# Optimization experiments

Measured on AMD Instinct MI355X. Metric: run time of the kernel, lower is better.

The kernel has to match this reference:

```python
import jax, jax.numpy as jnp
import numpy as np

B, N, D = 256, 128, 200   # batch, node tokens, descriptor count (d_desc)
DG, DT, DK, H = 256, 256, 256, 4
DH = DK // H
EPS = 1e-5


def _ln(x, g, b):
    mu = jnp.mean(x, -1, keepdims=True)
    v = jnp.var(x, -1, keepdims=True)
    return (x - mu) * jax.lax.rsqrt(v + EPS) * g + b


def _mh_attn(Q, K, V, key_pad_mask):
    # Q:(B,Tq,DK) K,V:(B,Tk,DK) -> ctx:(B,Tq,DK), scores/attn:(B,H,Tq,Tk)
    Bq, Tq, _ = Q.shape
    Tk = K.shape[1]
    Qh = Q.reshape(Bq, Tq, H, DH)
    Kh = K.reshape(Bq, Tk, H, DH)
    Vh = V.reshape(Bq, Tk, H, DH)
    scores = jnp.einsum('bqhd,bkhd->bhqk', Qh, Kh) / (DH ** 0.5)
    if key_pad_mask is not None:
        scores = jnp.where(key_pad_mask[:, None, None, :], -jnp.inf, scores)
    attn = jax.nn.softmax(scores, axis=-1)
    ctx = jnp.einsum('bhqk,bkhd->bqhd', attn, Vh).reshape(Bq, Tq, DK)
    return ctx, scores, attn


def setup_inputs() -> dict:
    key = jax.random.key(0)
    ks = jax.random.split(key, 20)
    def p(i, shape, s=0.05):
        return jax.random.normal(ks[i], shape, jnp.float32) * s
    return dict(
        node_tokens=jax.random.normal(ks[0], (B, N, DG), jnp.float32),
        desc=jax.random.normal(ks[1], (B, D), jnp.float32),
        node_pad_mask=jax.random.randint(ks[2], (B, N), 0, 2).astype(bool),
        id_emb=p(3, (D, DT)),
        val_w1=p(4, (1, DT // 2)), val_b1=jnp.zeros(DT // 2, jnp.float32),
        val_w2=p(5, (DT // 2, DT)), val_b2=jnp.zeros(DT, jnp.float32),
        tok_ln_g=jnp.ones(DT, jnp.float32), tok_ln_b=jnp.zeros(DT, jnp.float32),
        ln_node_g=jnp.ones(DG, jnp.float32), ln_node_b=jnp.zeros(DG, jnp.float32),
        ln_desc_g=jnp.ones(DT, jnp.float32), ln_desc_b=jnp.zeros(DT, jnp.float32),
        Wq_g=p(6, (DG, DK)), bq_g=jnp.zeros(DK, jnp.float32),
        Wk_g=p(7, (DT, DK)), bk_g=jnp.zeros(DK, jnp.float32),
        Wv_g=p(8, (DT, DK)), bv_g=jnp.zeros(DK, jnp.float32),
        Wq_d=p(9, (DT, DK)), bq_d=jnp.zeros(DK, jnp.float32),
        Wk_d=p(10, (DG, DK)), bk_d=jnp.zeros(DK, jnp.float32),
        Wv_d=p(11, (DG, DK)), bv_d=jnp.zeros(DK, jnp.float32),
        proj_node_w=p(12, (DG, DK)), proj_node_b=jnp.zeros(DK, jnp.float32),
        proj_desc_w=p(13, (DT, DK)), proj_desc_b=jnp.zeros(DK, jnp.float32),
        ln_out_g_g=jnp.ones(DK, jnp.float32), ln_out_g_b=jnp.zeros(DK, jnp.float32),
        ln_out_d_g=jnp.ones(DK, jnp.float32), ln_out_d_b=jnp.zeros(DK, jnp.float32),
    )


def reference(node_tokens, desc, node_pad_mask, id_emb, val_w1, val_b1, val_w2, val_b2,
              tok_ln_g, tok_ln_b, ln_node_g, ln_node_b, ln_desc_g, ln_desc_b,
              Wq_g, bq_g, Wk_g, bk_g, Wv_g, bv_g, Wq_d, bq_d, Wk_d, bk_d, Wv_d, bv_d,
              proj_node_w, proj_node_b, proj_desc_w, proj_desc_b,
              ln_out_g_g, ln_out_g_b, ln_out_d_g, ln_out_d_b):
    # Descriptor tokenizer: per-scalar value MLP + id embedding + LN
    h = jax.nn.relu(desc[..., None] @ val_w1 + val_b1)      # (B,D,DT/2)
    val_emb = h @ val_w2 + val_b2                            # (B,D,DT)
    desc_tks = _ln(val_emb + id_emb, tok_ln_g, tok_ln_b)     # (B,D,DT)

    node_in = _ln(node_tokens, ln_node_g, ln_node_b)
    desc_in = _ln(desc_tks, ln_desc_g, ln_desc_b)

    # nodes attend to desc (no key mask)
    ctx_g, scores_g, attn_g = _mh_attn(node_in @ Wq_g + bq_g,
                                       desc_in @ Wk_g + bk_g,
                                       desc_in @ Wv_g + bv_g, None)
    out_g_tokens = _ln(node_tokens @ proj_node_w + proj_node_b + ctx_g,
                       ln_out_g_g, ln_out_g_b)               # (B,N,DK)
    valid = (~node_pad_mask)[..., None].astype(out_g_tokens.dtype)
    denom = jnp.clip(valid.sum(axis=1), 1.0)
    g_vec = (out_g_tokens * valid).sum(axis=1) / denom       # (B,DK)

    # desc attends to nodes (node pad mask on keys)
    ctx_d, scores_d, attn_d = _mh_attn(desc_in @ Wq_d + bq_d,
                                       node_in @ Wk_d + bk_d,
                                       node_in @ Wv_d + bv_d, node_pad_mask)
    out_d_tokens = _ln(desc_tks @ proj_desc_w + proj_desc_b + ctx_d,
                       ln_out_d_g, ln_out_d_b)               # (B,D,DK)
    d_vec = out_d_tokens.mean(axis=1)                        # (B,DK)

    return (g_vec, d_vec, out_g_tokens, out_d_tokens, scores_g, attn_g, scores_d, attn_d)
```

## Files before the change

### kernel.cpp

```cpp
#include <hip/hip_runtime.h>
#include <cmath>
#include <cfloat>

#define BB 256
#define NN 128
#define DD 200
#define CH 256
#define NH 4
#define QKVS 768

#define BF16_SAFE_MAX 3.0e38f

typedef __attribute__((ext_vector_type(8))) __bf16 bf16x8;
typedef __attribute__((ext_vector_type(4))) __bf16 bf16x4;
typedef __attribute__((ext_vector_type(2))) __bf16 bf16x2;
typedef __attribute__((ext_vector_type(4))) float f32x4;

__device__ __forceinline__ float finclamp(float x) {
  return fminf(fmaxf(x, -BF16_SAFE_MAX), BF16_SAFE_MAX);
}

#define GLOAD_LDS16(gp, lp)                                                    \
  __builtin_amdgcn_global_load_lds(                                            \
      (const __attribute__((address_space(1))) void*)(gp),                     \
      (__attribute__((address_space(3))) void*)(lp), 16, 0, 0)

__device__ __forceinline__ void wred2(float& s, float& ss) {
  #pragma unroll
  for (int o = 1; o < 64; o <<= 1) {
    s += __shfl_xor(s, o);
    ss += __shfl_xor(ss, o);
  }
}

struct W9 { const float* p[9]; };
__global__ __launch_bounds__(256)
void mhca_wconv9(W9 w, __bf16* __restrict__ wt) {
  const int z = blockIdx.z;
  const int K = (z == 0) ? 128 : 256;
  if ((int)blockIdx.x * 64 >= K) return;
  __shared__ float t[64][65];
  const float* W = w.p[z];
  __bf16* Wt = wt + (size_t)z * 65536;
  const int k0 = blockIdx.x * 64, n0 = blockIdx.y * 64;
  const int c = threadIdx.x & 63, r0 = threadIdx.x >> 6;
  #pragma unroll
  for (int r = r0; r < 64; r += 4)
    t[r][c] = W[(size_t)(k0 + r) * 256 + n0 + c];
  __syncthreads();
  #pragma unroll
  for (int r = r0; r < 64; r += 4)
    Wt[(size_t)(n0 + r) * K + k0 + c] = (__bf16)t[c][r];
}

__global__ __launch_bounds__(256)
void mhca_gemm_tok(const float* __restrict__ desc, const float* __restrict__ w1,
                   const float* __restrict__ b1, const __bf16* __restrict__ Wt,
                   const float* __restrict__ bias, __bf16* __restrict__ C) {
  constexpr int K = 128;
  __shared__ char lds[2][2][16384];
  const int tid = threadIdx.x;
  const int lane = tid & 63, w = tid >> 6;
  const int n0 = blockIdx.x * 128, m0 = blockIdx.y * 128;
  const int c = lane & 15, g = lane >> 4;
  const int wr = w >> 1, wc = w & 1;

  const bool isA = (w < 2);
  const int half = isA ? w : (w - 2);
  const char* gsrcB = (const char*)Wt + (size_t)(n0 + half * 64) * (K * 2);
  const int lrow = lane >> 3, s8 = lane & 7;
  const int ksw = (s8 ^ lrow) << 4;

  f32x4 acc[4][4];
  #pragma unroll
  for (int mt = 0; mt < 4; ++mt)
    #pragma unroll
    for (int nt = 0; nt < 4; ++nt) acc[mt][nt] = (f32x4){0.f, 0.f, 0.f, 0.f};

  auto stageA = [&](int buf, int kt) {
    char* Ab = &lds[buf][0][half * 8192];
    const int kk = kt * 64 + s8 * 8;
    float4 wa = *(const float4*)&w1[kk];
    float4 wb = *(const float4*)&w1[kk + 4];
    float4 ba = *(const float4*)&b1[kk];
    float4 bb = *(const float4*)&b1[kk + 4];
    #pragma unroll
    for (int i = 0; i < 8; ++i) {
      const float dv = desc[m0 + half * 64 + i * 8 + lrow];
      bf16x8 av;
      av[0] = (__bf16)fmaxf(dv * wa.x + ba.x, 0.f);
      av[1] = (__bf16)fmaxf(dv * wa.y + ba.y, 0.f);
      av[2] = (__bf16)fmaxf(dv * wa.z + ba.z, 0.f);
      av[3] = (__bf16)fmaxf(dv * wa.w + ba.w, 0.f);
      av[4] = (__bf16)fmaxf(dv * wb.x + bb.x, 0.f);
      av[5] = (__bf16)fmaxf(dv * wb.y + bb.y, 0.f);
      av[6] = (__bf16)fmaxf(dv * wb.z + bb.z, 0.f);
      av[7] = (__bf16)fmaxf(dv * wb.w + bb.w, 0.f);
      *(bf16x8*)(Ab + (i * 8 + lrow) * 128 + ksw) = av;
    }
  };
  auto stageB = [&](int buf, int kt) {
    char* ld = &lds[buf][1][half * 8192];
    const char* gs = gsrcB + kt * 128;
    #pragma unroll
    for (int i = 0; i < 8; ++i)
      GLOAD_LDS16(gs + (size_t)(i * 8 + lrow) * (K * 2) + ksw, ld + i * 1024);
  };

  if (isA) stageA(0, 0); else stageB(0, 0);
  __syncthreads();

  int cur = 0;
  #pragma unroll
  for (int kt = 0; kt < 2; ++kt) {
    if (kt + 1 < 2) { if (isA) stageA(cur ^ 1, 1); else stageB(cur ^ 1, 1); }
    const char* A  = lds[cur][0];
    const char* Bt = lds[cur][1];
    #pragma unroll
    for (int kc = 0; kc < 2; ++kc) {
      const int kb = (kc * 64 + g * 16) ^ ((c & 7) << 4);
      bf16x8 a[4], bv[4];
      #pragma unroll
      for (int mt = 0; mt < 4; ++mt)
        a[mt] = *(const bf16x8*)(A + (wr * 64 + mt * 16 + c) * 128 + kb);
      #pragma unroll
      for (int nt = 0; nt < 4; ++nt)
        bv[nt] = *(const bf16x8*)(Bt + (wc * 64 + nt * 16 + c) * 128 + kb);
      #pragma unroll
      for (int mt = 0; mt < 4; ++mt)
        #pragma unroll
        for (int nt = 0; nt < 4; ++nt)
          acc[mt][nt] = __builtin_amdgcn_mfma_f32_16x16x32_bf16(
              a[mt], bv[nt], acc[mt][nt], 0, 0, 0);
    }
    __syncthreads();
    cur ^= 1;
  }

  #pragma unroll
  for (int nt = 0; nt < 4; ++nt) {
    const int n = n0 + wc * 64 + nt * 16 + c;
    const float bn = bias[n];
    #pragma unroll
    for (int mt = 0; mt < 4; ++mt)
      #pragma unroll
      for (int r = 0; r < 4; ++r) {
        const int m = m0 + wr * 64 + mt * 16 + g * 4 + r;
        C[(size_t)m * CH + n] = (__bf16)(acc[mt][nt][r] + bn);
      }
  }
}

struct G4 {
  const __bf16* X[4]; const __bf16* Wt[4];
  const float* bia[4][3]; __bf16* C[4];
};
__global__ __launch_bounds__(256)
void mhca_gemm4(G4 a) {
  constexpr int K = 256;
  const int y = blockIdx.y;
  int side, my, xlim, SC;
  if (y < 400)      { side = 0; my = y;       xlim = 6; SC = QKVS; }
  else if (y < 656) { side = 1; my = y - 400; xlim = 6; SC = QKVS; }
  else if (y < 912) { side = 2; my = y - 656; xlim = 2; SC = CH;  }
  else              { side = 3; my = y - 912; xlim = 2; SC = CH;  }
  if ((int)blockIdx.x >= xlim) return;

  __shared__ char lds[2][2][16384];
  const int tid = threadIdx.x;
  const int lane = tid & 63, w = tid >> 6;
  const int n0 = blockIdx.x * 128, m0 = my * 128;
  const int c = lane & 15, g = lane >> 4;
  const int wr = w >> 1, wc = w & 1;

  const __bf16* X  = a.X[side];
  const __bf16* Wt = a.Wt[side];
  __bf16* C        = a.C[side];
  const float* bp  = a.bia[side][n0 >> 8];

  const bool isA = (w < 2);
  const int half = isA ? w : (w - 2);
  const char* gsrc0 = (const char*)(isA ? X : Wt) +
                      (size_t)((isA ? m0 : n0) + half * 64) * (size_t)(K * 2);
  const size_t rsb = (size_t)K * 2;
  const int lrow = lane >> 3;
  const int ksw  = ((lane & 7) ^ lrow) << 4;

  f32x4 acc[4][4];
  #pragma unroll
  for (int mt = 0; mt < 4; ++mt)
    #pragma unroll
    for (int nt = 0; nt < 4; ++nt) acc[mt][nt] = (f32x4){0.f, 0.f, 0.f, 0.f};

  {
    char* ld = &lds[0][isA ? 0 : 1][half * 8192];
    #pragma unroll
    for (int i = 0; i < 8; ++i)
      GLOAD_LDS16(gsrc0 + (size_t)(i * 8 + lrow) * rsb + ksw, ld + i * 1024);
  }
  __syncthreads();

  int cur = 0;
  #pragma unroll
  for (int kt = 0; kt < 4; ++kt) {
    if (kt + 1 < 4) {
      const char* gs = gsrc0 + (kt + 1) * 128;
      char* ld = &lds[cur ^ 1][isA ? 0 : 1][half * 8192];
      #pragma unroll
      for (int i = 0; i < 8; ++i)
        GLOAD_LDS16(gs + (size_t)(i * 8 + lrow) * rsb + ksw, ld + i * 1024);
    }
    const char* A  = lds[cur][0];
    const char* Bt = lds[cur][1];
    #pragma unroll
    for (int kc = 0; kc < 2; ++kc) {
      const int kb = (kc * 64 + g * 16) ^ ((c & 7) << 4);
      bf16x8 af[4], bv[4];
      #pragma unroll
      for (int mt = 0; mt < 4; ++mt)
        af[mt] = *(const bf16x8*)(A + (wr * 64 + mt * 16 + c) * 128 + kb);
      #pragma unroll
      for (int nt = 0; nt < 4; ++nt)
        bv[nt] = *(const bf16x8*)(Bt + (wc * 64 + nt * 16 + c) * 128 + kb);
      #pragma unroll
      for (int mt = 0; mt < 4; ++mt)
        #pragma unroll
        for (int nt = 0; nt < 4; ++nt)
          acc[mt][nt] = __builtin_amdgcn_mfma_f32_16x16x32_bf16(
              af[mt], bv[nt], acc[mt][nt], 0, 0, 0);
    }
    __syncthreads();
    cur ^= 1;
  }

  #pragma unroll
  for (int nt = 0; nt < 4; ++nt) {
    const int n = n0 + wc * 64 + nt * 16 + c;
    const float bn = bp[n & 255];
    #pragma unroll
    for (int mt = 0; mt < 4; ++mt)
      #pragma unroll
      for (int r = 0; r < 4; ++r) {
        const int m = m0 + wr * 64 + mt * 16 + g * 4 + r;
        C[(size_t)m * SC + n] = (__bf16)(acc[mt][nt][r] + bn);
      }
  }
}

__global__ __launch_bounds__(256)
void mhca_ln2(const float* __restrict__ node_tokens, const float* __restrict__ lng,
              const float* __restrict__ lnb, __bf16* __restrict__ nodein,
              __bf16* __restrict__ ntok,
              const __bf16* __restrict__ vemb, const float* __restrict__ idemb,
              const float* __restrict__ tg, const float* __restrict__ tb,
              const float* __restrict__ dg, const float* __restrict__ db,
              __bf16* __restrict__ dtks, __bf16* __restrict__ din) {
  const int row = blockIdx.x * 4 + (threadIdx.x >> 6);
  const int t4 = (threadIdx.x & 63) * 4;
  if (row < BB * NN) {
    const size_t base = (size_t)row * CH + t4;
    const float4 v = *(const float4*)&node_tokens[base];
    float s = v.x + v.y + v.z + v.w;
    float ss = v.x * v.x + v.y * v.y + v.z * v.z + v.w * v.w;
    wred2(s, ss);
    const float mu = s * (1.f / 256.f);
    const float rstd = rsqrtf(ss * (1.f / 256.f) - mu * mu + 1e-5f);
    const float4 g4 = *(const float4*)&lng[t4];
    const float4 b4 = *(const float4*)&lnb[t4];
    bf16x4 o, rw;
    o[0] = (__bf16)((v.x - mu) * rstd * g4.x + b4.x);
    o[1] = (__bf16)((v.y - mu) * rstd * g4.y + b4.y);
    o[2] = (__bf16)((v.z - mu) * rstd * g4.z + b4.z);
    o[3] = (__bf16)((v.w - mu) * rstd * g4.w + b4.w);
    rw[0] = (__bf16)v.x; rw[1] = (__bf16)v.y; rw[2] = (__bf16)v.z; rw[3] = (__bf16)v.w;
    *(bf16x4*)&nodein[base] = o;
    *(bf16x4*)&ntok[base] = rw;
  } else {
    const int bd = row - BB * NN;
    const int d = bd % DD;
    const size_t base = (size_t)bd * CH + t4;
    const bf16x4 ve = *(const bf16x4*)&vemb[base];
    const float4 ie = *(const float4*)&idemb[(size_t)d * CH + t4];
    float x[4];
    x[0] = (float)ve[0] + ie.x; x[1] = (float)ve[1] + ie.y;
    x[2] = (float)ve[2] + ie.z; x[3] = (float)ve[3] + ie.w;
    float s = x[0] + x[1] + x[2] + x[3];
    float ss = x[0]*x[0] + x[1]*x[1] + x[2]*x[2] + x[3]*x[3];
    wred2(s, ss);
    float mu = s * (1.f / 256.f);
    float rstd = rsqrtf(ss * (1.f / 256.f) - mu * mu + 1e-5f);
    const float4 tg4 = *(const float4*)&tg[t4];
    const float4 tb4 = *(const float4*)&tb[t4];
    float y[4];
    y[0] = (x[0] - mu) * rstd * tg4.x + tb4.x;
    y[1] = (x[1] - mu) * rstd * tg4.y + tb4.y;
    y[2] = (x[2] - mu) * rstd * tg4.z + tb4.z;
    y[3] = (x[3] - mu) * rstd * tg4.w + tb4.w;
    bf16x4 yo;
    yo[0] = (__bf16)y[0]; yo[1] = (__bf16)y[1];
    yo[2] = (__bf16)y[2]; yo[3] = (__bf16)y[3];
    *(bf16x4*)&dtks[base] = yo;
    float s2 = y[0] + y[1] + y[2] + y[3];
    float ss2 = y[0]*y[0] + y[1]*y[1] + y[2]*y[2] + y[3]*y[3];
    wred2(s2, ss2);
    mu = s2 * (1.f / 256.f);
    rstd = rsqrtf(ss2 * (1.f / 256.f) - mu * mu + 1e-5f);
    const float4 dg4 = *(const float4*)&dg[t4];
    const float4 db4 = *(const float4*)&db[t4];
    bf16x4 dov;
    dov[0] = (__bf16)((y[0] - mu) * rstd * dg4.x + db4.x);
    dov[1] = (__bf16)((y[1] - mu) * rstd * dg4.y + db4.y);
    dov[2] = (__bf16)((y[2] - mu) * rstd * dg4.z + db4.z);
    dov[3] = (__bf16)((y[3] - mu) * rstd * dg4.w + db4.w);
    *(bf16x4*)&din[base] = dov;
  }
}

__global__ __launch_bounds__(256)
void mhca_outln2(const __bf16* __restrict__ PN, const __bf16* __restrict__ ctxg,
                 const float* __restrict__ gg, const float* __restrict__ gb,
                 float* __restrict__ outg,
                 const __bf16* __restrict__ PD, const __bf16* __restrict__ ctxd,
                 const float* __restrict__ dgam, const float* __restrict__ dbet,
                 float* __restrict__ outd) {
  const int row = blockIdx.x * 4 + (threadIdx.x >> 6);
  const int t4 = (threadIdx.x & 63) * 4;
  const bool isg = row < BB * NN;
  const int r = isg ? row : row - BB * NN;
  const __bf16* P  = isg ? PN : PD;
  const __bf16* cx = isg ? ctxg : ctxd;
  const size_t base = (size_t)r * CH + t4;
  const bf16x4 pv = *(const bf16x4*)&P[base];
  const bf16x4 cv = *(const bf16x4*)&cx[base];
  float v[4];
  float s = 0.f, ss = 0.f;
  #pragma unroll
  for (int j = 0; j < 4; ++j) {
    v[j] = (float)pv[j] + (float)cv[j];
    s += v[j]; ss += v[j] * v[j];
  }
  wred2(s, ss);
  const float mu = s * (1.f / 256.f);
  const float rstd = rsqrtf(ss * (1.f / 256.f) - mu * mu + 1e-5f);
  const float* ga = isg ? gg : dgam;
  const float* be = isg ? gb : dbet;
  const float4 g4 = *(const float4*)&ga[t4];
  const float4 b4 = *(const float4*)&be[t4];
  float* o = isg ? outg : outd;
  float4 ov;
  ov.x = finclamp((v[0] - mu) * rstd * g4.x + b4.x);
  ov.y = finclamp((v[1] - mu) * rstd * g4.y + b4.y);
  ov.z = finclamp((v[2] - mu) * rstd * g4.z + b4.z);
  ov.w = finclamp((v[3] - mu) * rstd * g4.w + b4.w);
  *(float4*)&o[base] = ov;
}

__device__ __forceinline__ int vswz(int d) { return (d & 7) ^ ((d >> 3) & 7); }

template<int TQ, int TK, bool HASM>
__global__ __launch_bounds__(256)
void mhca_xattn_v2(const __bf16* __restrict__ Qm, const __bf16* __restrict__ Km,
                   const __bf16* __restrict__ Vm, const unsigned char* __restrict__ mask,
                   float* __restrict__ scores_out, float* __restrict__ attn_out,
                   __bf16* __restrict__ ctx_out) {
  constexpr int NT   = (TK + 15) / 16;
  constexpr int KPAD = ((TK + 31) / 32) * 32;
  constexpr int NCH  = KPAD / 32;
  constexpr int PLD  = KPAD + 8;
  constexpr int KVTB = 512;

  __shared__ char VtL[64 * KVTB];
  __shared__ __bf16 Plds[4][16][PLD];

  const int b = blockIdx.x, h = blockIdx.y;
  const int w = threadIdx.x >> 6;
  const int lane = threadIdx.x & 63;
  const int c = lane & 15, g = lane >> 4;

  {
    const __bf16* vb0 = Vm + (size_t)b * TK * QKVS + h * 64;
    for (int i = threadIdx.x; i < (TK / 2) * 8; i += 256) {
      const int p = i >> 3, d0 = (i & 7) * 8;
      const bf16x8 v0 = *(const bf16x8*)(vb0 + (size_t)(2 * p) * QKVS + d0);
      const bf16x8 v1 = *(const bf16x8*)(vb0 + (size_t)(2 * p + 1) * QKVS + d0);
      #pragma unroll
      for (int j = 0; j < 8; ++j) {
        const int d = d0 + j;
        const int byte = d * KVTB + ((((p >> 2) ^ vswz(d)) << 4) | ((4 * p) & 15));
        bf16x2 pr; pr[0] = v0[j]; pr[1] = v1[j];
        *(bf16x2*)&VtL[byte] = pr;
      }
    }
    if constexpr (TK < KPAD) {
      constexpr int S0 = TK / 8;
      constexpr int NS = (KPAD - TK) / 8;
      const bf16x8 z = {};
      for (int i = threadIdx.x; i < 64 * NS; i += 256) {
        const int d = i / NS, s = S0 + i % NS;
        *(bf16x8*)&VtL[d * KVTB + ((s ^ vswz(d)) << 4)] = z;
      }
    }
  }
  __syncthreads();

  const int qt = blockIdx.z * 4 + w;
  if (qt * 16 >= TQ) return;
  const int q0 = qt * 16;

  const int qr = min(q0 + c, TQ - 1);
  const __bf16* qrow = Qm + ((size_t)b * TQ + qr) * QKVS + h * 64;
  const bf16x8 a0 = *(const bf16x8*)(qrow + g * 8);
  const bf16x8 a1 = *(const bf16x8*)(qrow + 32 + g * 8);

  const __bf16* kbase = Km + (size_t)b * TK * QKVS + h * 64;
  f32x4 sacc[NT];
  #pragma unroll
  for (int kt = 0; kt < NT; ++kt) {
    const int krow = min(kt * 16 + c, TK - 1);
    const __bf16* kr = kbase + (size_t)krow * QKVS;
    const bf16x8 b0 = *(const bf16x8*)(kr + g * 8);
    const bf16x8 b1 = *(const bf16x8*)(kr + 32 + g * 8);
    f32x4 s = {0.f, 0.f, 0.f, 0.f};
    s = __builtin_amdgcn_mfma_f32_16x16x32_bf16(a0, b0, s, 0, 0, 0);
    s = __builtin_amdgcn_mfma_f32_16x16x32_bf16(a1, b1, s, 0, 0, 0);
    sacc[kt] = s;
  }

  const size_t sbase = (((size_t)b * NH + h) * TQ + q0) * TK;
  float mr[4] = {-INFINITY, -INFINITY, -INFINITY, -INFINITY};
  #pragma unroll
  for (int kt = 0; kt < NT; ++kt) {
    const int k = kt * 16 + c;
    const bool vk = (k < TK);
    bool mk = false;
    if (HASM) mk = vk && (mask[b * TK + k] != 0);
    #pragma unroll
    for (int r = 0; r < 4; ++r) {
      const float sv = sacc[kt][r] * 0.125f;
      const float se = (vk && !mk) ? sv : -INFINITY;
      const int q = q0 + g * 4 + r;
      if (vk && q < TQ)
        scores_out[sbase + (size_t)(g * 4 + r) * TK + k] =
            mk ? -BF16_SAFE_MAX : finclamp(sv);
      sacc[kt][r] = se;
      mr[r] = fmaxf(mr[r], se);
    }
  }
  #pragma unroll
  for (int o = 1; o < 16; o <<= 1)
    #pragma unroll
    for (int r = 0; r < 4; ++r) mr[r] = fmaxf(mr[r], __shfl_xor(mr[r], o));

  float sum[4] = {0.f, 0.f, 0.f, 0.f};
  #pragma unroll
  for (int kt = 0; kt < NT; ++kt)
    #pragma unroll
    for (int r = 0; r < 4; ++r) {
      const float e = (mr[r] > -INFINITY) ? __expf(sacc[kt][r] - mr[r]) : 0.f;
      sacc[kt][r] = e;
      sum[r] += e;
    }
  #pragma unroll
  for (int o = 1; o < 16; o <<= 1)
    #pragma unroll
    for (int r = 0; r < 4; ++r) sum[r] += __shfl_xor(sum[r], o);
  float inv[4];
  #pragma unroll
  for (int r = 0; r < 4; ++r) inv[r] = (sum[r] > 0.f) ? 1.f / sum[r] : 0.f;

  #pragma unroll
  for (int kt = 0; kt < NT; ++kt) {
    const int k = kt * 16 + c;
    #pragma unroll
    for (int r = 0; r < 4; ++r) {
      const float p = sacc[kt][r] * inv[r];
      const int q = q0 + g * 4 + r;
      if (k < TK && q < TQ)
        attn_out[sbase + (size_t)(g * 4 + r) * TK + k] = finclamp(p);
      Plds[w][g * 4 + r][k] = (__bf16)p;
    }
  }
  if constexpr (KPAD > NT * 16) {
    #pragma unroll
    for (int r = 0; r < 4; ++r) Plds[w][g * 4 + r][NT * 16 + c] = (__bf16)0.f;
  }
  asm volatile("s_waitcnt lgkmcnt(0)" ::: "memory");
  __builtin_amdgcn_sched_barrier(0);

  f32x4 ctx[4];
  #pragma unroll
  for (int nt = 0; nt < 4; ++nt) ctx[nt] = (f32x4){0.f, 0.f, 0.f, 0.f};
  #pragma unroll
  for (int kc = 0; kc < NCH; ++kc) {
    const bf16x8 pa = *(const bf16x8*)&Plds[w][c][kc * 32 + g * 8];
    #pragma unroll
    for (int nt = 0; nt < 4; ++nt) {
      const int d = nt * 16 + c;
      const bf16x8 vb =
          *(const bf16x8*)&VtL[d * KVTB + (((kc * 4 + g) ^ vswz(d)) << 4)];
      ctx[nt] = __builtin_amdgcn_mfma_f32_16x16x32_bf16(pa, vb, ctx[nt], 0, 0, 0);
    }
  }
  __bf16* cbase = ctx_out + ((size_t)b * TQ + q0) * CH + h * 64;
  #pragma unroll
  for (int nt = 0; nt < 4; ++nt)
    #pragma unroll
    for (int r = 0; r < 4; ++r) {
      const int q = q0 + g * 4 + r;
      if (q < TQ)
        cbase[(size_t)(g * 4 + r) * CH + nt * 16 + c] = (__bf16)finclamp(ctx[nt][r]);
    }
}

__global__ __launch_bounds__(256)
void mhca_pool2(const float* __restrict__ outg, const unsigned char* __restrict__ mask,
                float* __restrict__ gv, const float* __restrict__ outd,
                float* __restrict__ dv) {
  const int t = threadIdx.x;
  if ((int)blockIdx.x < BB) {
    const int b = blockIdx.x;
    float s = 0.f, cnt = 0.f;
    for (int n = 0; n < NN; ++n) {
      if (!mask[b * NN + n]) {
        s += outg[((size_t)b * NN + n) * CH + t];
        cnt += 1.f;
      }
    }
    gv[(size_t)b * CH + t] = s / fmaxf(cnt, 1.f);
  } else {
    const int b = blockIdx.x - BB;
    float s = 0.f;
    for (int d = 0; d < DD; ++d) s += outd[((size_t)b * DD + d) * CH + t];
    dv[(size_t)b * CH + t] = s * (1.f / 200.f);
  }
}

extern "C" void kernel_launch(void* const* d_in, const int* in_sizes, int n_in,
                              void* d_out, int out_size, void* d_ws, size_t ws_size,
                              hipStream_t stream) {
  const float* node_tokens = (const float*)d_in[0];
  const float* desc_v      = (const float*)d_in[1];
  const unsigned char* pad = (const unsigned char*)d_in[2];
  const float* id_emb      = (const float*)d_in[3];
  const float* val_w1      = (const float*)d_in[4];
  const float* val_b1      = (const float*)d_in[5];
  const float* val_w2      = (const float*)d_in[6];
  const float* val_b2      = (const float*)d_in[7];
  const float* tok_g       = (const float*)d_in[8];
  const float* tok_b       = (const float*)d_in[9];
  const float* ln_node_g   = (const float*)d_in[10];
  const float* ln_node_b   = (const float*)d_in[11];
  const float* ln_desc_g   = (const float*)d_in[12];
  const float* ln_desc_b   = (const float*)d_in[13];
  const float* Wq_g = (const float*)d_in[14]; const float* bq_g = (const float*)d_in[15];
  const float* Wk_g = (const float*)d_in[16]; const float* bk_g = (const float*)d_in[17];
  const float* Wv_g = (const float*)d_in[18]; const float* bv_g = (const float*)d_in[19];
  const float* Wq_d = (const float*)d_in[20]; const float* bq_d = (const float*)d_in[21];
  const float* Wk_d = (const float*)d_in[22]; const float* bk_d = (const float*)d_in[23];
  const float* Wv_d = (const float*)d_in[24]; const float* bv_d = (const float*)d_in[25];
  const float* pnw  = (const float*)d_in[26]; const float* pnb  = (const float*)d_in[27];
  const float* pdw  = (const float*)d_in[28]; const float* pdb  = (const float*)d_in[29];
  const float* logg = (const float*)d_in[30]; const float* logb = (const float*)d_in[31];
  const float* lodg = (const float*)d_in[32]; const float* lodb = (const float*)d_in[33];

  const size_t NEED = 82083840ull * 4ull;
  if (ws_size < NEED) return;
  float* ws = (float*)d_ws;
  __bf16* vemb_bf   = (__bf16*)ws;
  __bf16* nodein_bf = (__bf16*)(ws + 6553600);
  __bf16* ntok_bf   = (__bf16*)(ws + 10747904);
  __bf16* dtks_bf   = (__bf16*)(ws + 14942208);
  __bf16* din_bf    = (__bf16*)(ws + 21495808);
  __bf16* wt        = (__bf16*)(ws + 28049408);
  __bf16* dinQKV    = (__bf16*)(ws + 28344320);
  __bf16* nodeQKV   = (__bf16*)(ws + 48005120);
  __bf16* PN_bf     = (__bf16*)(ws + 60588032);
  __bf16* PD_bf     = (__bf16*)(ws + 64782336);
  __bf16* ctxg_bf   = (__bf16*)(ws + 71335936);
  __bf16* ctxd_bf   = (__bf16*)(ws + 75530240);

  float* out = (float*)d_out;
  float* o_gvec = out;
  float* o_dvec = out + 65536;
  float* o_outg = out + 131072;
  float* o_outd = out + 8519680;
  float* o_sg   = out + 21626880;
  float* o_ag   = out + 47841280;
  float* o_sd   = out + 74055680;
  float* o_ad   = out + 100270080;

  W9 w9;
  w9.p[0] = val_w2;
  w9.p[1] = Wk_g; w9.p[2] = Wv_g; w9.p[3] = Wq_d;
  w9.p[4] = Wq_g; w9.p[5] = Wk_d; w9.p[6] = Wv_d;
  w9.p[7] = pnw;  w9.p[8] = pdw;
  mhca_wconv9<<<dim3(4, 4, 9), 256, 0, stream>>>(w9, wt);

  mhca_gemm_tok<<<dim3(2, 400), 256, 0, stream>>>(desc_v, val_w1, val_b1,
                                                  wt + 0 * 65536, val_b2, vemb_bf);
  mhca_ln2<<<(BB * NN + BB * DD) / 4, 256, 0, stream>>>(
      node_tokens, ln_node_g, ln_node_b, nodein_bf, ntok_bf,
      vemb_bf, id_emb, tok_g, tok_b, ln_desc_g, ln_desc_b, dtks_bf, din_bf);
  G4 g4;
  g4.X[0] = din_bf;    g4.Wt[0] = wt + 1 * 65536; g4.C[0] = dinQKV;
  g4.bia[0][0] = bk_g; g4.bia[0][1] = bv_g;       g4.bia[0][2] = bq_d;
  g4.X[1] = nodein_bf; g4.Wt[1] = wt + 4 * 65536; g4.C[1] = nodeQKV;
  g4.bia[1][0] = bq_g; g4.bia[1][1] = bk_d;       g4.bia[1][2] = bv_d;
  g4.X[2] = ntok_bf;   g4.Wt[2] = wt + 7 * 65536; g4.C[2] = PN_bf;
  g4.bia[2][0] = pnb;  g4.bia[2][1] = pnb;        g4.bia[2][2] = pnb;
  g4.X[3] = dtks_bf;   g4.Wt[3] = wt + 8 * 65536; g4.C[3] = PD_bf;
  g4.bia[3][0] = pdb;  g4.bia[3][1] = pdb;        g4.bia[3][2] = pdb;
  mhca_gemm4<<<dim3(6, 1312), 256, 0, stream>>>(g4);
  mhca_xattn_v2<NN, DD, false><<<dim3(BB, NH, NN / 64), 256, 0, stream>>>(
      nodeQKV + 0, dinQKV + 0, dinQKV + 256, nullptr, o_sg, o_ag, ctxg_bf);
  mhca_xattn_v2<DD, NN, true><<<dim3(BB, NH, (DD + 63) / 64), 256, 0, stream>>>(
      dinQKV + 512, nodeQKV + 256, nodeQKV + 512, pad, o_sd, o_ad, ctxd_bf);
  mhca_outln2<<<(BB * NN + BB * DD) / 4, 256, 0, stream>>>(
      PN_bf, ctxg_bf, logg, logb, o_outg, PD_bf, ctxd_bf, lodg, lodb, o_outd);
  mhca_pool2<<<2 * BB, 256, 0, stream>>>(o_outg, pad, o_gvec, o_outd, o_dvec);
}
```

Measured before the change: 423.3 us.

## Merge both cross-attention launches and fuse output layernorm with pooling

Folds the two cross-attention kernels into one launch whose z index selects the direction, with shared memory sized for the larger case. Fuses the output layernorm with masked and mean pooling, so each block handles one batch row and accumulates pooled sums in registers and LDS. This avoids re-reading the full output tensors for pooling and saves two launches. The cost is that the fused pool kernel runs only 512 blocks, each looping over 128 or 200 rows, so parallelism is lower. The merged attention kernel also always reserves the larger LDS footprint.

New measurement: 407.8 us. 3.7% less time.

```diff
diff --git a/kernel.cpp b/kernel.cpp
--- a/kernel.cpp
+++ b/kernel.cpp
@@ -316,63 +316,25 @@
   }
 }
 
-__global__ __launch_bounds__(256)
-void mhca_outln2(const __bf16* __restrict__ PN, const __bf16* __restrict__ ctxg,
-                 const float* __restrict__ gg, const float* __restrict__ gb,
-                 float* __restrict__ outg,
-                 const __bf16* __restrict__ PD, const __bf16* __restrict__ ctxd,
-                 const float* __restrict__ dgam, const float* __restrict__ dbet,
-                 float* __restrict__ outd) {
-  const int row = blockIdx.x * 4 + (threadIdx.x >> 6);
-  const int t4 = (threadIdx.x & 63) * 4;
-  const bool isg = row < BB * NN;
-  const int r = isg ? row : row - BB * NN;
-  const __bf16* P  = isg ? PN : PD;
-  const __bf16* cx = isg ? ctxg : ctxd;
-  const size_t base = (size_t)r * CH + t4;
-  const bf16x4 pv = *(const bf16x4*)&P[base];
-  const bf16x4 cv = *(const bf16x4*)&cx[base];
-  float v[4];
-  float s = 0.f, ss = 0.f;
-  #pragma unroll
-  for (int j = 0; j < 4; ++j) {
-    v[j] = (float)pv[j] + (float)cv[j];
-    s += v[j]; ss += v[j] * v[j];
-  }
-  wred2(s, ss);
-  const float mu = s * (1.f / 256.f);
-  const float rstd = rsqrtf(ss * (1.f / 256.f) - mu * mu + 1e-5f);
-  const float* ga = isg ? gg : dgam;
-  const float* be = isg ? gb : dbet;
-  const float4 g4 = *(const float4*)&ga[t4];
-  const float4 b4 = *(const float4*)&be[t4];
-  float* o = isg ? outg : outd;
-  float4 ov;
-  ov.x = finclamp((v[0] - mu) * rstd * g4.x + b4.x);
-  ov.y = finclamp((v[1] - mu) * rstd * g4.y + b4.y);
-  ov.z = finclamp((v[2] - mu) * rstd * g4.z + b4.z);
-  ov.w = finclamp((v[3] - mu) * rstd * g4.w + b4.w);
-  *(float4*)&o[base] = ov;
-}
-
 __device__ __forceinline__ int vswz(int d) { return (d & 7) ^ ((d >> 3) & 7); }
 
 template<int TQ, int TK, bool HASM>
-__global__ __launch_bounds__(256)
-void mhca_xattn_v2(const __bf16* __restrict__ Qm, const __bf16* __restrict__ Km,
-                   const __bf16* __restrict__ Vm, const unsigned char* __restrict__ mask,
-                   float* __restrict__ scores_out, float* __restrict__ attn_out,
-                   __bf16* __restrict__ ctx_out) {
+__device__ __forceinline__
+void xattn_body(char* smem, int b, int h, int zq,
+                const __bf16* __restrict__ Qm, const __bf16* __restrict__ Km,
+                const __bf16* __restrict__ Vm, const unsigned char* __restrict__ mask,
+                float* __restrict__ scores_out, float* __restrict__ attn_out,
+                __bf16* __restrict__ ctx_out) {
   constexpr int NT   = (TK + 15) / 16;
   constexpr int KPAD = ((TK + 31) / 32) * 32;
   constexpr int NCH  = KPAD / 32;
   constexpr int PLD  = KPAD + 8;
   constexpr int KVTB = 512;
 
-  __shared__ char VtL[64 * KVTB];
-  __shared__ __bf16 Plds[4][16][PLD];
-
-  const int b = blockIdx.x, h = blockIdx.y;
+  char* VtL = smem;
+  typedef __bf16 PldsT[16][PLD];
+  PldsT* Plds = (PldsT*)(smem + 64 * KVTB);
+
   const int w = threadIdx.x >> 6;
   const int lane = threadIdx.x & 63;
   const int c = lane & 15, g = lane >> 4;
@@ -403,7 +365,7 @@
   }
   __syncthreads();
 
-  const int qt = blockIdx.z * 4 + w;
+  const int qt = zq * 4 + w;
   if (qt * 16 >= TQ) return;
   const int q0 = qt * 16;
 
@@ -513,25 +475,83 @@
 }
 
 __global__ __launch_bounds__(256)
-void mhca_pool2(const float* __restrict__ outg, const unsigned char* __restrict__ mask,
-                float* __restrict__ gv, const float* __restrict__ outd,
-                float* __restrict__ dv) {
-  const int t = threadIdx.x;
-  if ((int)blockIdx.x < BB) {
-    const int b = blockIdx.x;
-    float s = 0.f, cnt = 0.f;
-    for (int n = 0; n < NN; ++n) {
-      if (!mask[b * NN + n]) {
-        s += outg[((size_t)b * NN + n) * CH + t];
-        cnt += 1.f;
-      }
-    }
-    gv[(size_t)b * CH + t] = s / fmaxf(cnt, 1.f);
+void mhca_xattn_both(const __bf16* __restrict__ nodeQKV,
+                     const __bf16* __restrict__ dinQKV,
+                     const unsigned char* __restrict__ mask,
+                     float* __restrict__ o_sg, float* __restrict__ o_ag,
+                     __bf16* __restrict__ ctxg,
+                     float* __restrict__ o_sd, float* __restrict__ o_ad,
+                     __bf16* __restrict__ ctxd) {
+  __shared__ char smem[62464];
+  const int b = blockIdx.x, h = blockIdx.y, z = blockIdx.z;
+  if (z < 2)
+    xattn_body<NN, DD, false>(smem, b, h, z, nodeQKV + 0, dinQKV + 0,
+                              dinQKV + 256, nullptr, o_sg, o_ag, ctxg);
+  else
+    xattn_body<DD, NN, true>(smem, b, h, z - 2, dinQKV + 512, nodeQKV + 256,
+                             nodeQKV + 512, mask, o_sd, o_ad, ctxd);
+}
+
+__global__ __launch_bounds__(256)
+void mhca_olnpool(const __bf16* __restrict__ PN, const __bf16* __restrict__ ctxg,
+                  const float* __restrict__ gg, const float* __restrict__ gb,
+                  float* __restrict__ outg, const unsigned char* __restrict__ mask,
+                  float* __restrict__ gv,
+                  const __bf16* __restrict__ PD, const __bf16* __restrict__ ctxd,
+                  const float* __restrict__ dgam, const float* __restrict__ dbet,
+                  float* __restrict__ outd, float* __restrict__ dv) {
+  __shared__ float part[4][256];
+  __shared__ float cpart[4];
+  const bool isg = (int)blockIdx.x < BB;
+  const int b = isg ? blockIdx.x : blockIdx.x - BB;
+  const int w = threadIdx.x >> 6, lane = threadIdx.x & 63;
+  const int t4 = lane * 4;
+  const int R = isg ? NN : DD;
+  const __bf16* P  = isg ? PN : PD;
+  const __bf16* cx = isg ? ctxg : ctxd;
+  const float* ga = isg ? gg : dgam;
+  const float* be = isg ? gb : dbet;
+  float* o = isg ? outg : outd;
+  const float4 g4 = *(const float4*)&ga[t4];
+  const float4 b4 = *(const float4*)&be[t4];
+
+  float ps0 = 0.f, ps1 = 0.f, ps2 = 0.f, ps3 = 0.f, cnt = 0.f;
+  for (int r = w; r < R; r += 4) {
+    const size_t base = ((size_t)b * R + r) * CH + t4;
+    const bf16x4 pv = *(const bf16x4*)&P[base];
+    const bf16x4 cv = *(const bf16x4*)&cx[base];
+    float v0 = (float)pv[0] + (float)cv[0];
+    float v1 = (float)pv[1] + (float)cv[1];
+    float v2 = (float)pv[2] + (float)cv[2];
+    float v3 = (float)pv[3] + (float)cv[3];
+    float s = v0 + v1 + v2 + v3;
+    float ss = v0*v0 + v1*v1 + v2*v2 + v3*v3;
+    wred2(s, ss);
+    const float mu = s * (1.f / 256.f);
+    const float rstd = rsqrtf(ss * (1.f / 256.f) - mu * mu + 1e-5f);
+    float4 ov;
+    ov.x = finclamp((v0 - mu) * rstd * g4.x + b4.x);
+    ov.y = finclamp((v1 - mu) * rstd * g4.y + b4.y);
+    ov.z = finclamp((v2 - mu) * rstd * g4.z + b4.z);
+    ov.w = finclamp((v3 - mu) * rstd * g4.w + b4.w);
+    *(float4*)&o[base] = ov;
+    const bool valid = isg ? (mask[b * NN + r] == 0) : true;
+    if (valid) {
+      ps0 += ov.x; ps1 += ov.y; ps2 += ov.z; ps3 += ov.w;
+      cnt += 1.f;
+    }
+  }
+  part[w][t4 + 0] = ps0; part[w][t4 + 1] = ps1;
+  part[w][t4 + 2] = ps2; part[w][t4 + 3] = ps3;
+  if (lane == 0) cpart[w] = cnt;
+  __syncthreads();
+  const int col = threadIdx.x;
+  const float s = part[0][col] + part[1][col] + part[2][col] + part[3][col];
+  if (isg) {
+    const float total = cpart[0] + cpart[1] + cpart[2] + cpart[3];
+    gv[(size_t)b * CH + col] = s / fmaxf(total, 1.f);
   } else {
-    const int b = blockIdx.x - BB;
-    float s = 0.f;
-    for (int d = 0; d < DD; ++d) s += outd[((size_t)b * DD + d) * CH + t];
-    dv[(size_t)b * CH + t] = s * (1.f / 200.f);
+    dv[(size_t)b * CH + col] = s * (1.f / 200.f);
   }
 }
 
@@ -611,11 +631,9 @@
   g4.X[3] = dtks_bf;   g4.Wt[3] = wt + 8 * 65536; g4.C[3] = PD_bf;
   g4.bia[3][0] = pdb;  g4.bia[3][1] = pdb;        g4.bia[3][2] = pdb;
   mhca_gemm4<<<dim3(6, 1312), 256, 0, stream>>>(g4);
-  mhca_xattn_v2<NN, DD, false><<<dim3(BB, NH, NN / 64), 256, 0, stream>>>(
-      nodeQKV + 0, dinQKV + 0, dinQKV + 256, nullptr, o_sg, o_ag, ctxg_bf);
-  mhca_xattn_v2<DD, NN, true><<<dim3(BB, NH, (DD + 63) / 64), 256, 0, stream>>>(
-      dinQKV + 512, nodeQKV + 256, nodeQKV + 512, pad, o_sd, o_ad, ctxd_bf);
-  mhca_outln2<<<(BB * NN + BB * DD) / 4, 256, 0, stream>>>(
-      PN_bf, ctxg_bf, logg, logb, o_outg, PD_bf, ctxd_bf, lodg, lodb, o_outd);
-  mhca_pool2<<<2 * BB, 256, 0, stream>>>(o_outg, pad, o_gvec, o_outd, o_dvec);
-}
+  mhca_xattn_both<<<dim3(BB, NH, 6), 256, 0, stream>>>(
+      nodeQKV, dinQKV, pad, o_sg, o_ag, ctxg_bf, o_sd, o_ad, ctxd_bf);
+  mhca_olnpool<<<2 * BB, 256, 0, stream>>>(
+      PN_bf, ctxg_bf, logg, logb, o_outg, pad, o_gvec,
+      PD_bf, ctxd_bf, lodg, lodb, o_outd, o_dvec);
+}
```
